# Performance work log

Hardware: AMD Instinct MI355X
Metric: run time of the kernel (lower is better)

The kernel has to match this reference:

```python
import jax, jax.numpy as jnp
import numpy as np

B, SP, SH, H = 32, 256, 256, 512
D = 2 * H       # input feature dim (2*hidden_size)
E = H // 2      # per-liner output dim
FD = 4 * H      # fusion linear dim
EPS = 1e-13


def setup_inputs() -> dict:
    key = jax.random.key(0)
    ks = jax.random.split(key, 8)
    s = 0.02
    return dict(
        premise_batch=jax.random.normal(ks[0], (B, SP, D), jnp.float32),
        hypothesis_batch=jax.random.normal(ks[1], (B, SH, D), jnp.float32),
        premise_mask=jax.random.randint(ks[2], (B, SP), 0, 2).astype(jnp.int32),
        hypothesis_mask=jax.random.randint(ks[3], (B, SH), 0, 2).astype(jnp.int32),
        W8=jax.random.normal(ks[4], (8, D, E), jnp.float32) * s,   # liner1..8 weights (in,out)
        B8=jnp.zeros((8, E), jnp.float32),
        Wl=jax.random.normal(ks[5], (8 * E, FD), jnp.float32) * s,  # self.liner
        bl=jnp.zeros((FD,), jnp.float32),
        Wp=jax.random.normal(ks[6], (7 * D, H), jnp.float32) * s,   # self._projection
        bp=jnp.zeros((H,), jnp.float32),
    )


def masked_softmax(logits, mask):
    # ESIM-style: multiply logits by mask, softmax, re-mask, renormalize.
    m = mask[:, None, :]                        # (b,1,kv)
    r = jax.nn.softmax(logits * m, axis=-1) * m
    return r / (r.sum(axis=-1, keepdims=True) + EPS)


def fuse(x, imp_self, imp_inter, W8, B8, Wl, bl):
    # x: (b,s,D); imp_*: (b,s,1). Eight modulated views -> liner1..8 -> concat -> liner+ReLU.
    a1 = imp_self * imp_inter
    a2 = imp_self + imp_inter
    a3 = jnp.maximum(imp_self, imp_inter)
    x1 = x * imp_self
    x2 = x * imp_inter
    mx = jnp.maximum(x1, x2)
    feats = jnp.stack([x * a1, x * a2, x * a3, mx,
                       x * (a1 + 1.0), x * (a2 + 1.0), x * (a3 + 1.0), mx + x], 0)  # (8,b,s,D)
    h = jnp.einsum('kbsd,kde->kbse', feats, W8) + B8[:, None, None, :]              # (8,b,s,E)
    cat = jnp.moveaxis(h, 0, 2).reshape(x.shape[0], x.shape[1], 8 * E)              # concat order 1..8
    return jax.nn.relu(cat @ Wl + bl)           # dropout is identity in eval mode


def reference(premise_batch, hypothesis_batch, premise_mask, hypothesis_mask,
              W8, B8, Wl, bl, Wp, bp):
    pm = premise_mask.astype(jnp.float32)
    hm = hypothesis_mask.astype(jnp.float32)
    scale = 1.0 / jnp.sqrt(jnp.float32(premise_batch.shape[-1]))

    sim = jnp.einsum('bpd,bhd->bph', premise_batch, hypothesis_batch) * scale
    ph = masked_softmax(sim, hm)                               # (b,Sp,Sh)
    hp = masked_softmax(sim.transpose(0, 2, 1), pm)            # (b,Sh,Sp)
    att_p = jnp.einsum('bph,bhd->bpd', ph, hypothesis_batch) * pm[:, :, None]
    att_h = jnp.einsum('bhp,bpd->bhd', hp, premise_batch) * hm[:, :, None]

    sp_attn = jax.nn.softmax(jnp.einsum('bpd,bqd->bpq', premise_batch, premise_batch) * scale, axis=-1)
    sh_attn = jax.nn.softmax(jnp.einsum('bpd,bqd->bpq', hypothesis_batch, hypothesis_batch) * scale, axis=-1)
    self_p = sp_attn @ premise_batch
    self_h = sh_attn @ hypothesis_batch

    imp_p = sp_attn.sum(axis=-2)[..., None]        # (b,Sp,1)
    imp_h = sh_attn.sum(axis=-2)[..., None]        # (b,Sh,1)
    inter_imp_h = ph.sum(axis=-2)[..., None]       # (b,Sh,1)
    inter_imp_p = hp.sum(axis=-2)[..., None]       # (b,Sp,1)

    p_all = fuse(premise_batch, imp_p, inter_imp_p, W8, B8, Wl, bl)
    h_all = fuse(hypothesis_batch, imp_h, inter_imp_h, W8, B8, Wl, bl)

    enh_p = jnp.concatenate([premise_batch, att_p, self_p, p_all,
                             premise_batch * att_p, premise_batch - att_p], axis=-1)
    enh_h = jnp.concatenate([hypothesis_batch, att_h, self_h, h_all,
                             hypothesis_batch * att_h, hypothesis_batch - att_h], axis=-1)
    out_p = jax.nn.relu(enh_p @ Wp + bp)
    out_h = jax.nn.relu(enh_h @ Wp + bp)
    return out_p, out_h
```

## Files before the change

kernel.cpp:

```cpp
#include <hip/hip_runtime.h>
#include <hip/hip_bf16.h>
#include <cmath>

#define BB 32
#define SS 256
#define DD 1024
#define EE 256
#define FDIM 2048
#define HH 512
#define KOUT6 (6 * 1024)
#define NROW (BB * SS)
#define NROW2 (2 * NROW)
#define SIMSZ ((size_t)BB * SS * SS)

static constexpr float SCALE = 1.0f / 32.0f;
static constexpr float EPSF  = 1e-13f;

typedef __attribute__((ext_vector_type(8))) short bf16x8;
typedef __attribute__((ext_vector_type(4))) float f32x4;

__device__ inline float4 ld4(const float* p) { return *(const float4*)p; }
__device__ inline ushort f2b(float f) {
    uint x = __float_as_uint(f);
    x += 0x7fffu + ((x >> 16) & 1u);
    return (ushort)(x >> 16);
}
__device__ inline float b2f(ushort u) { return __uint_as_float(((uint)u) << 16); }
__device__ inline bf16x8 cvt8(const float* v) {
    bf16x8 r;
#pragma unroll
    for (int j = 0; j < 8; ++j) r[j] = (short)f2b(v[j]);
    return r;
}
__device__ inline void b2f8(bf16x8 v, float* o) {
#pragma unroll
    for (int j = 0; j < 8; ++j) o[j] = b2f((ushort)v[j]);
}
__device__ inline bf16x8 ldf8(const float* p) {
    const float4 u0 = ld4(p), u1 = ld4(p + 4);
    float v[8] = {u0.x, u0.y, u0.z, u0.w, u1.x, u1.y, u1.z, u1.w};
    return cvt8(v);
}

__device__ inline int swz_orig_2d() {
    const int n   = blockIdx.y * gridDim.x + blockIdx.x;
    const int tot = gridDim.x * gridDim.y;
    return (n & 7) * (tot >> 3) + (n >> 3);
}
__device__ inline int swz_orig_3d() {
    const int n   = (blockIdx.z * gridDim.y + blockIdx.y) * gridDim.x + blockIdx.x;
    const int tot = gridDim.x * gridDim.y * gridDim.z;
    return (n & 7) * (tot >> 3) + (n >> 3);
}

__global__ __launch_bounds__(256)
void tpose_cvt_k(const float* __restrict__ in, ushort* __restrict__ out,
                 int K, int N, size_t inStride, size_t outStride) {
    __shared__ float T[32][33];
    const float* ib = in  + (size_t)blockIdx.z * inStride;
    ushort*      ob = out + (size_t)blockIdx.z * outStride;
    const int k0 = blockIdx.x * 32, n0 = blockIdx.y * 32;
    const int tx = threadIdx.x & 31, ty = threadIdx.x >> 5;
#pragma unroll
    for (int i = 0; i < 4; ++i) T[ty + 8 * i][tx] = ib[(size_t)(k0 + ty + 8 * i) * N + n0 + tx];
    __syncthreads();
#pragma unroll
    for (int i = 0; i < 4; ++i)
        ob[(size_t)(n0 + ty + 8 * i) * K + k0 + tx] = f2b(T[tx][ty + 8 * i]);
}

__global__ __launch_bounds__(256)
void tpose_wp_k(const float* __restrict__ Wp, ushort* __restrict__ out) {
    __shared__ float T[32][33];
    const int k0 = blockIdx.x * 32, n0 = blockIdx.y * 32;
    const int tx = threadIdx.x & 31, ty = threadIdx.x >> 5;
#pragma unroll
    for (int i = 0; i < 4; ++i) {
        const int k = k0 + ty + 8 * i, n = n0 + tx;
        float v = Wp[(size_t)k * HH + n];
        if (k < DD)           v += Wp[(size_t)(k + 6 * DD) * HH + n];
        else if (k < 2 * DD)  v -= Wp[(size_t)(k + 5 * DD) * HH + n];
        T[ty + 8 * i][tx] = v;
    }
    __syncthreads();
#pragma unroll
    for (int i = 0; i < 4; ++i)
        out[(size_t)(n0 + ty + 8 * i) * KOUT6 + k0 + tx] = f2b(T[tx][ty + 8 * i]);
}

__global__ __launch_bounds__(256)
void prep_xprod_k(const float* __restrict__ P, const float* __restrict__ H,
                  const ushort* __restrict__ attAb,
                  ushort* __restrict__ Xb, ushort* __restrict__ prodb) {
    const int idx = blockIdx.x * 256 + threadIdx.x;
    const int row = idx >> 7, chunk = idx & 127;
    const size_t off = (size_t)row * DD + chunk * 8;
    const float* X = (row < NROW) ? (P + off) : (H + off - (size_t)NROW * DD);
    const float4 x0 = ld4(X), x1 = ld4(X + 4);
    float xv[8] = {x0.x, x0.y, x0.z, x0.w, x1.x, x1.y, x1.z, x1.w};
    float av[8];
    b2f8(*(const bf16x8*)&attAb[off], av);
    float pv[8];
#pragma unroll
    for (int j = 0; j < 8; ++j) pv[j] = xv[j] * av[j];
    *(bf16x8*)&Xb[off]    = cvt8(xv);
    *(bf16x8*)&prodb[off] = cvt8(pv);
}

__global__ __launch_bounds__(256)
void reduce_out_k(float* __restrict__ out, const float* __restrict__ p1,
                  const float* __restrict__ bp) {
    const int gid = blockIdx.x * 256 + threadIdx.x;
    const size_t o = (size_t)gid * 4;
    const float4 a = ld4(&out[o]);
    const float4 b = ld4(&p1[o]);
    const float4 bv = ld4(&bp[(int)(o & 511)]);
    *(float4*)&out[o] = make_float4(fmaxf(a.x + b.x + bv.x, 0.f),
                                    fmaxf(a.y + b.y + bv.y, 0.f),
                                    fmaxf(a.z + b.z + bv.z, 0.f),
                                    fmaxf(a.w + b.w + bv.w, 0.f));
}

__global__ __launch_bounds__(256)
void softmax4_k(ushort* __restrict__ simPH, ushort* __restrict__ simPHT,
                ushort* __restrict__ simPP, ushort* __restrict__ simHH,
                const int* __restrict__ pma, const int* __restrict__ hma) {
    const int job = blockIdx.y;
    ushort* buf = job == 0 ? simPH : job == 1 ? simPHT : job == 2 ? simPP : simHH;
    const int* mask = job == 0 ? hma : job == 1 ? pma : nullptr;
    const int w = threadIdx.x >> 6, lane = threadIdx.x & 63;
    const int row = blockIdx.x * 4 + w;
    const int b = row >> 8;
    ushort* rp = buf + (size_t)row * SS + lane * 4;
    ushort4 u = *(const ushort4*)rp;
    float z[4], mj[4];
    const ushort uv[4] = {u.x, u.y, u.z, u.w};
#pragma unroll
    for (int c = 0; c < 4; ++c) {
        const float v = b2f(uv[c]);
        float m = 1.f;
        if (mask) m = (float)mask[b * SS + lane * 4 + c];
        mj[c] = m; z[c] = v * m;
    }
    float M = fmaxf(fmaxf(z[0], z[1]), fmaxf(z[2], z[3]));
#pragma unroll
    for (int off = 1; off < 64; off <<= 1) M = fmaxf(M, __shfl_xor(M, off));
    float e[4], r[4], sz = 0.f, sr = 0.f;
#pragma unroll
    for (int c = 0; c < 4; ++c) {
        e[c] = expf(z[c] - M);
        r[c] = e[c] * mj[c];
        sz += e[c]; sr += r[c];
    }
#pragma unroll
    for (int off = 1; off < 64; off <<= 1) {
        sz += __shfl_xor(sz, off);
        sr += __shfl_xor(sr, off);
    }
    ushort4 o;
    if (mask) {
        const float d = 1.f / (sr + EPSF * sz);
        o.x = f2b(r[0] * d); o.y = f2b(r[1] * d); o.z = f2b(r[2] * d); o.w = f2b(r[3] * d);
    } else {
        const float d = 1.f / sz;
        o.x = f2b(e[0] * d); o.y = f2b(e[1] * d); o.z = f2b(e[2] * d); o.w = f2b(e[3] * d);
    }
    *(ushort4*)rp = o;
}

__global__ __launch_bounds__(256)
void colsum_p1_k(const ushort* __restrict__ simPP, const ushort* __restrict__ simHH,
                 const ushort* __restrict__ simPHT, const ushort* __restrict__ simPH,
                 float* __restrict__ pbuf) {
    const int job = blockIdx.y, b = blockIdx.x, rc = blockIdx.z, j = threadIdx.x;
    const ushort* src = job == 0 ? simPP : job == 1 ? simHH : job == 2 ? simPHT : simPH;
    const ushort* Mb = src + (size_t)b * SS * SS + (size_t)rc * 32 * SS;
    float s = 0.f;
#pragma unroll 4
    for (int i = 0; i < 32; ++i) s += b2f(Mb[i * SS + j]);
    pbuf[(((size_t)job * BB + b) * 8 + rc) * SS + j] = s;
}

__global__ __launch_bounds__(256)
void colsum_p2_k(const float* __restrict__ pbuf,
                 float* __restrict__ impS, float* __restrict__ impI) {
    const int job = blockIdx.y, b = blockIdx.x, j = threadIdx.x;
    const float* pb = pbuf + ((size_t)job * BB + b) * 8 * SS;
    float s = 0.f;
#pragma unroll
    for (int rc = 0; rc < 8; ++rc) s += pb[rc * SS + j];
    float* dst = job == 0 ? impS : job == 1 ? impS + NROW : job == 2 ? impI : impI + NROW;
    dst[b * SS + j] = s;
}

#define LSWZ(kg, r) ((r) ^ ((kg) << 1))

#define MFMA_CORE()                                                                  \
    {                                                                                \
        bf16x8 afr[4], bfr[4];                                                       \
        _Pragma("unroll") for (int m = 0; m < 4; ++m)                                \
            afr[m] = *(const bf16x8*)As[kq][LSWZ(kq, wr + m * 16 + fr)];             \
        _Pragma("unroll") for (int n = 0; n < 4; ++n)                                \
            bfr[n] = *(const bf16x8*)Bs[kq][LSWZ(kq, wc + n * 16 + fr)];             \
        _Pragma("unroll") for (int m = 0; m < 4; ++m)                                \
            _Pragma("unroll") for (int n = 0; n < 4; ++n)                            \
                acc[m][n] = __builtin_amdgcn_mfma_f32_16x16x32_bf16(                 \
                    afr[m], bfr[n], acc[m][n], 0, 0, 0);                             \
    }

#define MFMA_PREAMBLE()                                                              \
    const int tid = threadIdx.x;                                                     \
    const int lane = tid & 63;                                                       \
    const int w = tid >> 6;                                                          \
    const int wr = (w >> 1) * 64, wc = (w & 1) * 64;                                 \
    const int fr = lane & 15;                                                        \
    const int kq = lane >> 4;                                                        \
    const int rq = kq * 4;                                                           \
    f32x4 acc[4][4] = {};

__global__ __launch_bounds__(256)
void mfma_nt_k(const float* __restrict__ P, const float* __restrict__ H,
               ushort* __restrict__ simPH, ushort* __restrict__ simPHT,
               ushort* __restrict__ simPP, ushort* __restrict__ simHH) {
    __shared__ __align__(16) ushort As[4][128][8];
    __shared__ __align__(16) ushort Bs[4][128][8];
    int orig = swz_orig_3d();
    const int cb = orig & 1; orig >>= 1;
    const int rb = orig & 1; orig >>= 1;
    const int g = orig >> 5, b = orig & 31;
    const float* Au = ((g == 2) ? H : P) + (size_t)b * SS * DD;
    const float* Bu = ((g == 1) ? P : H) + (size_t)b * SS * DD;
    const int col0 = cb * 128, row0 = rb * 128;
    MFMA_PREAMBLE();
    for (int k0 = 0; k0 < DD; k0 += 32) {
        bf16x8 ar[2], br[2];
#pragma unroll
        for (int i = 0; i < 2; ++i) {
            const int cid = tid + i * 256, srow = cid >> 2, skc = (cid & 3) * 8;
            ar[i] = ldf8(&Au[(size_t)(row0 + srow) * DD + k0 + skc]);
            br[i] = ldf8(&Bu[(size_t)(col0 + srow) * DD + k0 + skc]);
        }
        __syncthreads();
#pragma unroll
        for (int i = 0; i < 2; ++i) {
            const int cid = tid + i * 256, kg = cid & 3, rr = LSWZ(kg, cid >> 2);
            *(bf16x8*)As[kg][rr] = ar[i];
            *(bf16x8*)Bs[kg][rr] = br[i];
        }
        __syncthreads();
        MFMA_CORE();
    }
    ushort* Cb = (g == 0 ? simPH : g == 1 ? simPP : simHH) + (size_t)b * SS * SS;
#pragma unroll
    for (int m = 0; m < 4; ++m)
#pragma unroll
        for (int n = 0; n < 4; ++n) {
            const int c = col0 + wc + n * 16 + fr;
            const int r0 = row0 + wr + m * 16 + rq;
#pragma unroll
            for (int r = 0; r < 4; ++r) Cb[(size_t)(r0 + r) * SS + c] = f2b(acc[m][n][r] * SCALE);
            if (g == 0) {
                ushort* Tb = simPHT + (size_t)b * SS * SS;
                ushort4 t;
                t.x = f2b(acc[m][n][0] * SCALE); t.y = f2b(acc[m][n][1] * SCALE);
                t.z = f2b(acc[m][n][2] * SCALE); t.w = f2b(acc[m][n][3] * SCALE);
                *(ushort4*)&Tb[(size_t)c * SS + r0] = t;
            }
        }
}

__global__ __launch_bounds__(256)
void mfma_att_k(const ushort* __restrict__ ph, const ushort* __restrict__ hp,
                const ushort* __restrict__ spA, const ushort* __restrict__ shA,
                const ushort* __restrict__ PbT, const ushort* __restrict__ HbT,
                const int* __restrict__ pma, const int* __restrict__ hma,
                ushort* __restrict__ attAb, ushort* __restrict__ selfAb) {
    __shared__ __align__(16) ushort As[4][128][8];
    __shared__ __align__(16) ushort Bs[4][128][8];
    int orig = swz_orig_3d();
    const int x = orig & 7; orig >>= 3;
    const int y = orig & 1; orig >>= 1;
    const int g = orig >> 5, b = orig & 31;
    const ushort* W  = (g == 0 ? ph : g == 1 ? hp : g == 2 ? spA : shA) + (size_t)b * SS * SS;
    const ushort* BT = ((g == 0 || g == 3) ? HbT : PbT) + (size_t)b * DD * SS;
    const int* rmask = g == 0 ? pma + b * SS : g == 1 ? hma + b * SS : nullptr;
    const int side = (g == 1 || g == 3);
    ushort* Ob = (g < 2 ? attAb : selfAb) + ((size_t)side * NROW + (size_t)b * SS) * DD;
    const int col0 = x * 128, row0 = y * 128;
    MFMA_PREAMBLE();
    for (int k0 = 0; k0 < SS; k0 += 32) {
        bf16x8 ar[2], br[2];
#pragma unroll
        for (int i = 0; i < 2; ++i) {
            const int cid = tid + i * 256, srow = cid >> 2, skc = (cid & 3) * 8;
            ar[i] = *(const bf16x8*)&W [(size_t)(row0 + srow) * SS + k0 + skc];
            br[i] = *(const bf16x8*)&BT[(size_t)(col0 + srow) * SS + k0 + skc];
        }
        __syncthreads();
#pragma unroll
        for (int i = 0; i < 2; ++i) {
            const int cid = tid + i * 256, kg = cid & 3, rr = LSWZ(kg, cid >> 2);
            *(bf16x8*)As[kg][rr] = ar[i];
            *(bf16x8*)Bs[kg][rr] = br[i];
        }
        __syncthreads();
        MFMA_CORE();
    }
#pragma unroll
    for (int m = 0; m < 4; ++m)
#pragma unroll
        for (int n = 0; n < 4; ++n) {
            const int c = col0 + wc + n * 16 + fr;
#pragma unroll
            for (int r = 0; r < 4; ++r) {
                const int rr = row0 + wr + m * 16 + rq + r;
                const float mm = rmask ? (float)rmask[rr] : 1.0f;
                Ob[(size_t)rr * DD + c] = f2b(acc[m][n][r] * mm);
            }
        }
}

__global__ __launch_bounds__(256)
void mfma_fuse_k(const float* __restrict__ P, const float* __restrict__ H,
                 const float* __restrict__ impS, const float* __restrict__ impI,
                 const ushort* __restrict__ W8T, const float* __restrict__ B8v,
                 ushort* __restrict__ catb) {
    __shared__ __align__(16) ushort As[4][128][8];
    __shared__ __align__(16) ushort Bs[4][128][8];
    const int orig = swz_orig_2d();
    const int cb = orig & 15, rb = orig >> 4;
    const int kf = cb >> 1, e0 = (cb & 1) * 128, row0 = rb * 128;
    const float* X = (row0 < NROW) ? P : H;
    const int rbase = (row0 < NROW) ? row0 : row0 - NROW;
    MFMA_PREAMBLE();
    const ushort* Wk = W8T + (size_t)kf * EE * DD;

    int srow_[2]; float sA[2], iA[2], cf[2];
#pragma unroll
    for (int i = 0; i < 2; ++i) {
        const int cid = tid + i * 256;
        srow_[i] = cid >> 2;
        const float s_ = impS[row0 + srow_[i]], i_ = impI[row0 + srow_[i]];
        sA[i] = s_; iA[i] = i_;
        float c = 0.f;
        switch (kf) {
            case 0: c = s_ * i_;             break;
            case 1: c = s_ + i_;             break;
            case 2: c = fmaxf(s_, i_);       break;
            case 4: c = s_ * i_ + 1.f;       break;
            case 5: c = s_ + i_ + 1.f;       break;
            case 6: c = fmaxf(s_, i_) + 1.f; break;
            default: break;
        }
        cf[i] = c;
    }
    for (int k0 = 0; k0 < DD; k0 += 32) {
        bf16x8 ar[2], br[2];
#pragma unroll
        for (int i = 0; i < 2; ++i) {
            const int cid = tid + i * 256, skc = (cid & 3) * 8;
            const float* src = &X[(size_t)(rbase + srow_[i]) * DD + k0 + skc];
            const float4 u0 = ld4(src), u1 = ld4(src + 4);
            float v[8] = {u0.x, u0.y, u0.z, u0.w, u1.x, u1.y, u1.z, u1.w};
            if (kf == 3) {
#pragma unroll
                for (int j = 0; j < 8; ++j) v[j] = fmaxf(v[j] * sA[i], v[j] * iA[i]);
            } else if (kf == 7) {
#pragma unroll
                for (int j = 0; j < 8; ++j) v[j] = fmaxf(v[j] * sA[i], v[j] * iA[i]) + v[j];
            } else {
#pragma unroll
                for (int j = 0; j < 8; ++j) v[j] *= cf[i];
            }
            ar[i] = cvt8(v);
            br[i] = *(const bf16x8*)&Wk[(size_t)(e0 + srow_[i]) * DD + k0 + skc];
        }
        __syncthreads();
#pragma unroll
        for (int i = 0; i < 2; ++i) {
            const int cid = tid + i * 256, kg = cid & 3, rr = LSWZ(kg, cid >> 2);
            *(bf16x8*)As[kg][rr] = ar[i];
            *(bf16x8*)Bs[kg][rr] = br[i];
        }
        __syncthreads();
        MFMA_CORE();
    }
#pragma unroll
    for (int m = 0; m < 4; ++m)
#pragma unroll
        for (int n = 0; n < 4; ++n) {
            const int el = e0 + wc + n * 16 + fr;
            const float bv = B8v[kf * EE + el];
#pragma unroll
            for (int r = 0; r < 4; ++r) {
                const int rr = row0 + wr + m * 16 + rq + r;
                catb[(size_t)rr * FDIM + kf * EE + el] = f2b(acc[m][n][r] + bv);
            }
        }
}

__global__ __launch_bounds__(256)
void mfma_lin_k(const ushort* __restrict__ A, const ushort* __restrict__ BT,
                const float* __restrict__ bias, ushort* __restrict__ C) {
    __shared__ __align__(16) ushort As[4][128][8];
    __shared__ __align__(16) ushort Bs[4][128][8];
    const int orig = swz_orig_2d();
    const int col0 = (orig & 15) * 128, row0 = (orig >> 4) * 128;
    MFMA_PREAMBLE();
    for (int k0 = 0; k0 < FDIM; k0 += 32) {
        bf16x8 ar[2], br[2];
#pragma unroll
        for (int i = 0; i < 2; ++i) {
            const int cid = tid + i * 256, srow = cid >> 2, skc = (cid & 3) * 8;
            ar[i] = *(const bf16x8*)&A [(size_t)(row0 + srow) * FDIM + k0 + skc];
            br[i] = *(const bf16x8*)&BT[(size_t)(col0 + srow) * FDIM + k0 + skc];
        }
        __syncthreads();
#pragma unroll
        for (int i = 0; i < 2; ++i) {
            const int cid = tid + i * 256, kg = cid & 3, rr = LSWZ(kg, cid >> 2);
            *(bf16x8*)As[kg][rr] = ar[i];
            *(bf16x8*)Bs[kg][rr] = br[i];
        }
        __syncthreads();
        MFMA_CORE();
    }
#pragma unroll
    for (int m = 0; m < 4; ++m)
#pragma unroll
        for (int n = 0; n < 4; ++n) {
            const int c = col0 + wc + n * 16 + fr;
            const float bv = bias[c];
#pragma unroll
            for (int r = 0; r < 4; ++r) {
                const int rr = row0 + wr + m * 16 + rq + r;
                C[(size_t)rr * FDIM + c] = f2b(fmaxf(acc[m][n][r] + bv, 0.f));
            }
        }
}

__device__ inline void out_seg(int k0, const ushort* Xb, const ushort* attAb,
                               const ushort* selfAb, const ushort* pallb,
                               const ushort* prodb,
                               const ushort*& seg, int& pitch, int& kloc) {
    switch (k0 >> 10) {
        case 0:  seg = Xb;     pitch = DD;   kloc = k0;          break;
        case 1:  seg = attAb;  pitch = DD;   kloc = k0 - DD;     break;
        case 2:  seg = selfAb; pitch = DD;   kloc = k0 - 2 * DD; break;
        case 3:
        case 4:  seg = pallb;  pitch = FDIM; kloc = k0 - 3 * DD; break;
        default: seg = prodb;  pitch = DD;   kloc = k0 - 5 * DD; break;
    }
}

__global__ __launch_bounds__(256)
void mfma_out_k(const ushort* __restrict__ Xb, const ushort* __restrict__ attAb,
                const ushort* __restrict__ selfAb, const ushort* __restrict__ pallb,
                const ushort* __restrict__ prodb, const ushort* __restrict__ WpT,
                const float* __restrict__ bp, float* __restrict__ dst0,
                float* __restrict__ dst1, int kchunk, int finalize) {
    __shared__ __align__(16) ushort As[4][128][8];
    __shared__ __align__(16) ushort Bs[4][128][8];
    int orig = swz_orig_3d();
    const int x = orig & 3; orig >>= 2;
    const int y = orig & 127; orig >>= 7;
    const int z = orig;
    const int col0 = x * 128, row0 = y * 128;
    const int kbase = z * kchunk;
    float* dst = z == 0 ? dst0 : dst1;
    MFMA_PREAMBLE();
    for (int t = 0; t < kchunk / 32; ++t) {
        const int k0 = kbase + t * 32;
        const ushort* seg; int pitch, kloc;
        out_seg(k0, Xb, attAb, selfAb, pallb, prodb, seg, pitch, kloc);
        bf16x8 ar[2], br[2];
#pragma unroll
        for (int i = 0; i < 2; ++i) {
            const int cid = tid + i * 256, srow = cid >> 2, skc = (cid & 3) * 8;
            ar[i] = *(const bf16x8*)&seg[(size_t)(row0 + srow) * pitch + kloc + skc];
            br[i] = *(const bf16x8*)&WpT[(size_t)(col0 + srow) * KOUT6 + k0 + skc];
        }
        __syncthreads();
#pragma unroll
        for (int i = 0; i < 2; ++i) {
            const int cid = tid + i * 256, kg = cid & 3, rr = LSWZ(kg, cid >> 2);
            *(bf16x8*)As[kg][rr] = ar[i];
            *(bf16x8*)Bs[kg][rr] = br[i];
        }
        __syncthreads();
        MFMA_CORE();
    }
#pragma unroll
    for (int m = 0; m < 4; ++m)
#pragma unroll
        for (int n = 0; n < 4; ++n) {
            const int c = col0 + wc + n * 16 + fr;
            const float bv = finalize ? bp[c] : 0.f;
#pragma unroll
            for (int r = 0; r < 4; ++r) {
                const int rr = row0 + wr + m * 16 + rq + r;
                const float v = acc[m][n][r] + bv;
                dst[(size_t)rr * HH + c] = finalize ? fmaxf(v, 0.f) : v;
            }
        }
}

extern "C" void kernel_launch(void* const* d_in, const int* in_sizes, int n_in,
                              void* d_out, int out_size, void* d_ws, size_t ws_size,
                              hipStream_t stream) {
    const float* P   = (const float*)d_in[0];
    const float* Hb  = (const float*)d_in[1];
    const int*   pma = (const int*)d_in[2];
    const int*   hma = (const int*)d_in[3];
    const float* W8  = (const float*)d_in[4];
    const float* B8v = (const float*)d_in[5];
    const float* Wl  = (const float*)d_in[6];
    const float* bl  = (const float*)d_in[7];
    const float* Wp  = (const float*)d_in[8];
    const float* bp  = (const float*)d_in[9];

    char* base = (char*)d_ws;
    ushort* simPH  = (ushort*)base;
    ushort* simPHT = simPH  + SIMSZ;
    ushort* simPP  = simPHT + SIMSZ;
    ushort* simHH  = simPP  + SIMSZ;
    ushort* PbT    = simHH + SIMSZ;
    ushort* HbT    = PbT + (size_t)NROW * DD;
    ushort* catb   = (ushort*)base;
    ushort* Xb     = (ushort*)base;
    ushort* prodb  = Xb + (size_t)NROW2 * DD;
    char* cur = base + (size_t)NROW2 * FDIM * 2;
    auto alloc_f = [&](size_t n) { float*  p = (float*)cur;  cur += n * 4; return p; };
    auto alloc_u = [&](size_t n) { ushort* p = (ushort*)cur; cur += n * 2; return p; };
    float*  impS   = alloc_f(NROW2);
    float*  impI   = alloc_f(NROW2);
    ushort* attAb  = alloc_u((size_t)NROW2 * DD);
    ushort* selfAb = alloc_u((size_t)NROW2 * DD);
    ushort* pallb  = alloc_u((size_t)NROW2 * FDIM);
    ushort* WlT    = alloc_u((size_t)FDIM * FDIM);
    ushort* WpT    = alloc_u((size_t)HH * KOUT6);
    ushort* W8T    = alloc_u((size_t)8 * EE * DD);
    float*  pbuf   = alloc_f((size_t)4 * BB * 8 * SS);
    float*  part1  = alloc_f((size_t)NROW2 * HH);

    const size_t need_split = (size_t)((char*)(part1 + (size_t)NROW2 * HH) - base);
    const bool split = ws_size >= need_split;

    float* outp = (float*)d_out;
    const dim3 blk(256);

    tpose_cvt_k<<<dim3(8, 32, BB), blk, 0, stream>>>(P,  PbT, SS, DD, (size_t)SS * DD, (size_t)DD * SS);
    tpose_cvt_k<<<dim3(8, 32, BB), blk, 0, stream>>>(Hb, HbT, SS, DD, (size_t)SS * DD, (size_t)DD * SS);
    tpose_cvt_k<<<dim3(FDIM / 32, FDIM / 32, 1), blk, 0, stream>>>(Wl, WlT, FDIM, FDIM, 0, 0);
    tpose_wp_k<<<dim3(KOUT6 / 32, HH / 32, 1), blk, 0, stream>>>(Wp, WpT);
    tpose_cvt_k<<<dim3(DD / 32, EE / 32, 8), blk, 0, stream>>>(W8, W8T, DD, EE,
                                                               (size_t)DD * EE, (size_t)EE * DD);

    mfma_nt_k<<<dim3(2, 2, 96), blk, 0, stream>>>(P, Hb, simPH, simPHT, simPP, simHH);
    softmax4_k<<<dim3(NROW / 4, 4), blk, 0, stream>>>(simPH, simPHT, simPP, simHH, pma, hma);
    colsum_p1_k<<<dim3(BB, 4, 8), blk, 0, stream>>>(simPP, simHH, simPHT, simPH, pbuf);
    colsum_p2_k<<<dim3(BB, 4), blk, 0, stream>>>(pbuf, impS, impI);
    mfma_att_k<<<dim3(8, 2, 128), blk, 0, stream>>>(simPH, simPHT, simPP, simHH, PbT, HbT,
                                                    pma, hma, attAb, selfAb);

    mfma_fuse_k<<<dim3(16, 128), blk, 0, stream>>>(P, Hb, impS, impI, W8T, B8v, catb);
    mfma_lin_k<<<dim3(16, 128), blk, 0, stream>>>(catb, WlT, bl, pallb);
    prep_xprod_k<<<dim3(NROW2 * DD / 8 / 256), blk, 0, stream>>>(P, Hb, attAb, Xb, prodb);
    if (split) {
        mfma_out_k<<<dim3(4, 128, 2), blk, 0, stream>>>(Xb, attAb, selfAb, pallb, prodb,
                                                        WpT, bp, outp, part1, KOUT6 / 2, 0);
        reduce_out_k<<<dim3(NROW2 * HH / 4 / 256), blk, 0, stream>>>(outp, part1, bp);
    } else {
        mfma_out_k<<<dim3(4, 128, 1), blk, 0, stream>>>(Xb, attAb, selfAb, pallb, prodb,
                                                        WpT, bp, outp, outp, KOUT6, 1);
    }

    (void)in_sizes; (void)n_in; (void)out_size; (void)ws_size;
}
```

Before: 726.8 us.

## Stage bf16 GEMM tiles via global_load_lds direct-to-LDS loads

Replaces the register-staged global-to-LDS tile copies in the bf16-input GEMM kernels (attention, fusion-linear, weight side of liner, output projection) with global_load_lds 16-byte direct loads. The LDS layout becomes row-major [128][32] with an XOR swizzle on the 16-byte column chunk, and new fragment-read macros use that layout. The aim is to cut VGPR use and the VALU/ds_write instructions spent moving tiles through registers. Loads are still single-buffered with two barriers per k-step, so load latency is not overlapped, and the swizzle and wait handling must be exactly right.

```diff
diff --git a/kernel.cpp b/kernel.cpp
--- a/kernel.cpp
+++ b/kernel.cpp
@@ -40,6 +40,12 @@
     const float4 u0 = ld4(p), u1 = ld4(p + 4);
     float v[8] = {u0.x, u0.y, u0.z, u0.w, u1.x, u1.y, u1.z, u1.w};
     return cvt8(v);
+}
+
+typedef __attribute__((address_space(1))) const uchar gas_t;
+typedef __attribute__((address_space(3))) uchar las_t;
+__device__ inline void gll16(const ushort* g, ushort* l) {
+    __builtin_amdgcn_global_load_lds((gas_t*)g, (las_t*)l, 16, 0, 0);
 }
 
 __device__ inline int swz_orig_2d() {
@@ -194,18 +200,37 @@
 }
 
 #define LSWZ(kg, r) ((r) ^ ((kg) << 1))
-
-#define MFMA_CORE()                                                                  \
+#define FRAG_R(T, r) (*(const bf16x8*)T[kq][LSWZ(kq, r)])
+#define FRAG_G(T, r) (*(const bf16x8*)&T[r][(kq ^ ((r) & 3)) * 8])
+
+#define MFMA_TAIL(afr, bfr)                                                          \
+    _Pragma("unroll") for (int m = 0; m < 4; ++m)                                    \
+        _Pragma("unroll") for (int n = 0; n < 4; ++n)                                \
+            acc[m][n] = __builtin_amdgcn_mfma_f32_16x16x32_bf16(                     \
+                afr[m], bfr[n], acc[m][n], 0, 0, 0);
+
+#define MFMA_CORE_R()                                                                \
     {                                                                                \
         bf16x8 afr[4], bfr[4];                                                       \
-        _Pragma("unroll") for (int m = 0; m < 4; ++m)                                \
-            afr[m] = *(const bf16x8*)As[kq][LSWZ(kq, wr + m * 16 + fr)];             \
-        _Pragma("unroll") for (int n = 0; n < 4; ++n)                                \
-            bfr[n] = *(const bf16x8*)Bs[kq][LSWZ(kq, wc + n * 16 + fr)];             \
-        _Pragma("unroll") for (int m = 0; m < 4; ++m)                                \
-            _Pragma("unroll") for (int n = 0; n < 4; ++n)                            \
-                acc[m][n] = __builtin_amdgcn_mfma_f32_16x16x32_bf16(                 \
-                    afr[m], bfr[n], acc[m][n], 0, 0, 0);                             \
+        _Pragma("unroll") for (int m = 0; m < 4; ++m) afr[m] = FRAG_R(As, wr + m * 16 + fr); \
+        _Pragma("unroll") for (int n = 0; n < 4; ++n) bfr[n] = FRAG_R(Bs, wc + n * 16 + fr); \
+        MFMA_TAIL(afr, bfr)                                                          \
+    }
+
+#define MFMA_CORE_G()                                                                \
+    {                                                                                \
+        bf16x8 afr[4], bfr[4];                                                       \
+        _Pragma("unroll") for (int m = 0; m < 4; ++m) afr[m] = FRAG_G(As, wr + m * 16 + fr); \
+        _Pragma("unroll") for (int n = 0; n < 4; ++n) bfr[n] = FRAG_G(Bs, wc + n * 16 + fr); \
+        MFMA_TAIL(afr, bfr)                                                          \
+    }
+
+#define MFMA_CORE_RG()                                                               \
+    {                                                                                \
+        bf16x8 afr[4], bfr[4];                                                       \
+        _Pragma("unroll") for (int m = 0; m < 4; ++m) afr[m] = FRAG_R(As, wr + m * 16 + fr); \
+        _Pragma("unroll") for (int n = 0; n < 4; ++n) bfr[n] = FRAG_G(Bs, wc + n * 16 + fr); \
+        MFMA_TAIL(afr, bfr)                                                          \
     }
 
 #define MFMA_PREAMBLE()                                                              \
@@ -217,6 +242,17 @@
     const int kq = lane >> 4;                                                        \
     const int rq = kq * 4;                                                           \
     f32x4 acc[4][4] = {};
+
+#define GLL_STAGE2(seg, pitch, r0, kloc, T)                                          \
+    {                                                                                \
+        const int rl0_ = w * 32 + (lane >> 2);                                       \
+        const int cp_ = lane & 3;                                                    \
+        gll16((seg) + (size_t)((r0) + rl0_) * (pitch) + (kloc) + ((cp_ ^ (rl0_ & 3)) * 8), \
+              &T[w * 32][0]);                                                        \
+        const int rl1_ = rl0_ + 16;                                                  \
+        gll16((seg) + (size_t)((r0) + rl1_) * (pitch) + (kloc) + ((cp_ ^ (rl1_ & 3)) * 8), \
+              &T[w * 32 + 16][0]);                                                   \
+    }
 
 __global__ __launch_bounds__(256)
 void mfma_nt_k(const float* __restrict__ P, const float* __restrict__ H,
@@ -248,7 +284,7 @@
             *(bf16x8*)Bs[kg][rr] = br[i];
         }
         __syncthreads();
-        MFMA_CORE();
+        MFMA_CORE_R();
     }
     ushort* Cb = (g == 0 ? simPH : g == 1 ? simPP : simHH) + (size_t)b * SS * SS;
 #pragma unroll
@@ -275,8 +311,8 @@
                 const ushort* __restrict__ PbT, const ushort* __restrict__ HbT,
                 const int* __restrict__ pma, const int* __restrict__ hma,
                 ushort* __restrict__ attAb, ushort* __restrict__ selfAb) {
-    __shared__ __align__(16) ushort As[4][128][8];
-    __shared__ __align__(16) ushort Bs[4][128][8];
+    __shared__ __align__(16) ushort As[128][32];
+    __shared__ __align__(16) ushort Bs[128][32];
     int orig = swz_orig_3d();
     const int x = orig & 7; orig >>= 3;
     const int y = orig & 1; orig >>= 1;
@@ -289,22 +325,11 @@
     const int col0 = x * 128, row0 = y * 128;
     MFMA_PREAMBLE();
     for (int k0 = 0; k0 < SS; k0 += 32) {
-        bf16x8 ar[2], br[2];
-#pragma unroll
-        for (int i = 0; i < 2; ++i) {
-            const int cid = tid + i * 256, srow = cid >> 2, skc = (cid & 3) * 8;
-            ar[i] = *(const bf16x8*)&W [(size_t)(row0 + srow) * SS + k0 + skc];
-            br[i] = *(const bf16x8*)&BT[(size_t)(col0 + srow) * SS + k0 + skc];
-        }
-        __syncthreads();
-#pragma unroll
-        for (int i = 0; i < 2; ++i) {
-            const int cid = tid + i * 256, kg = cid & 3, rr = LSWZ(kg, cid >> 2);
-            *(bf16x8*)As[kg][rr] = ar[i];
-            *(bf16x8*)Bs[kg][rr] = br[i];
-        }
-        __syncthreads();
-        MFMA_CORE();
+        __syncthreads();
+        GLL_STAGE2(W,  SS, row0, k0, As);
+        GLL_STAGE2(BT, SS, col0, k0, Bs);
+        __syncthreads();
+        MFMA_CORE_G();
     }
 #pragma unroll
     for (int m = 0; m < 4; ++m)
@@ -326,7 +351,7 @@
                  const ushort* __restrict__ W8T, const float* __restrict__ B8v,
                  ushort* __restrict__ catb) {
     __shared__ __align__(16) ushort As[4][128][8];
-    __shared__ __align__(16) ushort Bs[4][128][8];
+    __shared__ __align__(16) ushort Bs[128][32];
     const int orig = swz_orig_2d();
     const int cb = orig & 15, rb = orig >> 4;
     const int kf = cb >> 1, e0 = (cb & 1) * 128, row0 = rb * 128;
@@ -355,7 +380,7 @@
         cf[i] = c;
     }
     for (int k0 = 0; k0 < DD; k0 += 32) {
-        bf16x8 ar[2], br[2];
+        bf16x8 ar[2];
 #pragma unroll
         for (int i = 0; i < 2; ++i) {
             const int cid = tid + i * 256, skc = (cid & 3) * 8;
@@ -373,17 +398,16 @@
                 for (int j = 0; j < 8; ++j) v[j] *= cf[i];
             }
             ar[i] = cvt8(v);
-            br[i] = *(const bf16x8*)&Wk[(size_t)(e0 + srow_[i]) * DD + k0 + skc];
-        }
-        __syncthreads();
+        }
+        __syncthreads();
+        GLL_STAGE2(Wk, DD, e0, k0, Bs);
 #pragma unroll
         for (int i = 0; i < 2; ++i) {
             const int cid = tid + i * 256, kg = cid & 3, rr = LSWZ(kg, cid >> 2);
             *(bf16x8*)As[kg][rr] = ar[i];
-            *(bf16x8*)Bs[kg][rr] = br[i];
-        }
-        __syncthreads();
-        MFMA_CORE();
+        }
+        __syncthreads();
+        MFMA_CORE_RG();
     }
 #pragma unroll
     for (int m = 0; m < 4; ++m)
@@ -402,28 +426,17 @@
 __global__ __launch_bounds__(256)
 void mfma_lin_k(const ushort* __restrict__ A, const ushort* __restrict__ BT,
                 const float* __restrict__ bias, ushort* __restrict__ C) {
-    __shared__ __align__(16) ushort As[4][128][8];
-    __shared__ __align__(16) ushort Bs[4][128][8];
+    __shared__ __align__(16) ushort As[128][32];
+    __shared__ __align__(16) ushort Bs[128][32];
     const int orig = swz_orig_2d();
     const int col0 = (orig & 15) * 128, row0 = (orig >> 4) * 128;
     MFMA_PREAMBLE();
     for (int k0 = 0; k0 < FDIM; k0 += 32) {
-        bf16x8 ar[2], br[2];
-#pragma unroll
-        for (int i = 0; i < 2; ++i) {
-            const int cid = tid + i * 256, srow = cid >> 2, skc = (cid & 3) * 8;
-            ar[i] = *(const bf16x8*)&A [(size_t)(row0 + srow) * FDIM + k0 + skc];
-            br[i] = *(const bf16x8*)&BT[(size_t)(col0 + srow) * FDIM + k0 + skc];
-        }
-        __syncthreads();
-#pragma unroll
-        for (int i = 0; i < 2; ++i) {
-            const int cid = tid + i * 256, kg = cid & 3, rr = LSWZ(kg, cid >> 2);
-            *(bf16x8*)As[kg][rr] = ar[i];
-            *(bf16x8*)Bs[kg][rr] = br[i];
-        }
-        __syncthreads();
-        MFMA_CORE();
+        __syncthreads();
+        GLL_STAGE2(A,  FDIM, row0, k0, As);
+        GLL_STAGE2(BT, FDIM, col0, k0, Bs);
+        __syncthreads();
+        MFMA_CORE_G();
     }
 #pragma unroll
     for (int m = 0; m < 4; ++m)
@@ -459,8 +472,8 @@
                 const ushort* __restrict__ prodb, const ushort* __restrict__ WpT,
                 const float* __restrict__ bp, float* __restrict__ dst0,
                 float* __restrict__ dst1, int kchunk, int finalize) {
-    __shared__ __align__(16) ushort As[4][128][8];
-    __shared__ __align__(16) ushort Bs[4][128][8];
+    __shared__ __align__(16) ushort As[128][32];
+    __shared__ __align__(16) ushort Bs[128][32];
     int orig = swz_orig_3d();
     const int x = orig & 3; orig >>= 2;
     const int y = orig & 127; orig >>= 7;
@@ -473,22 +486,11 @@
         const int k0 = kbase + t * 32;
         const ushort* seg; int pitch, kloc;
         out_seg(k0, Xb, attAb, selfAb, pallb, prodb, seg, pitch, kloc);
-        bf16x8 ar[2], br[2];
-#pragma unroll
-        for (int i = 0; i < 2; ++i) {
-            const int cid = tid + i * 256, srow = cid >> 2, skc = (cid & 3) * 8;
-            ar[i] = *(const bf16x8*)&seg[(size_t)(row0 + srow) * pitch + kloc + skc];
-            br[i] = *(const bf16x8*)&WpT[(size_t)(col0 + srow) * KOUT6 + k0 + skc];
-        }
-        __syncthreads();
-#pragma unroll
-        for (int i = 0; i < 2; ++i) {
-            const int cid = tid + i * 256, kg = cid & 3, rr = LSWZ(kg, cid >> 2);
-            *(bf16x8*)As[kg][rr] = ar[i];
-            *(bf16x8*)Bs[kg][rr] = br[i];
-        }
-        __syncthreads();
-        MFMA_CORE();
+        __syncthreads();
+        GLL_STAGE2(seg, pitch, row0, kloc, As);
+        GLL_STAGE2(WpT, KOUT6, col0, k0, Bs);
+        __syncthreads();
+        MFMA_CORE_G();
     }
 #pragma unroll
     for (int m = 0; m < 4; ++m)
```

Result: no change. 716.9 us (-1.4%).
